# Performance work log

Measured on AMD Instinct MI355X. Metric: run time of the kernel, lower is better.

Reference implementation:

```python
import jax, jax.numpy as jnp
import numpy as np

DIM = 1024
NUM_HEADS = 16
HEAD_DIM = DIM // NUM_HEADS
ROPE_THETA = 10000.0
SCALE = HEAD_DIM ** -0.5


def _apply_rope(x, cos, sin):
    # x: [B, H, S, head_dim]; cos/sin: [S, head_dim//2] (broadcast over B, H)
    x_even = x[..., 0::2]
    x_odd = x[..., 1::2]
    rot_even = x_even * cos - x_odd * sin
    rot_odd = x_even * sin + x_odd * cos
    # interleave back: stack on last axis then flatten, matching torch .stack(-1).flatten(-2)
    return jnp.stack([rot_even, rot_odd], axis=-1).reshape(x.shape)


def setup_inputs() -> dict:
    key = jax.random.key(0)
    k0, k1, k2 = jax.random.split(key, 3)
    B, S = 2, 2048
    x = jax.random.normal(k0, (B, S, DIM), dtype=jnp.float32)
    # small_init: std = sqrt(2 / (5*dim))
    qkv_w = jax.random.normal(k1, (3 * DIM, DIM), dtype=jnp.float32) * (2.0 / (5 * DIM)) ** 0.5
    qkv_b = jnp.zeros((3 * DIM,), dtype=jnp.float32)
    # wang_init: std = 2 / num_blocks / sqrt(dim) scaled
    out_w = jax.random.normal(k2, (DIM, DIM), dtype=jnp.float32) * (2.0 / DIM) ** 0.5 / 2.0
    out_b = jnp.zeros((DIM,), dtype=jnp.float32)
    return {"x": x, "qkv_w": qkv_w, "qkv_b": qkv_b, "out_w": out_w, "out_b": out_b, "window_size": 512}


def reference(x, qkv_w, qkv_b, out_w, out_b, window_size):
    B, S, D = x.shape
    qkv = x @ qkv_w.T + qkv_b                          # [B, S, 3D]
    qkv = qkv.reshape(B, S, 3, NUM_HEADS, HEAD_DIM).transpose(2, 0, 3, 1, 4)
    q, k, v = qkv[0], qkv[1], qkv[2]                   # each [B, H, S, hd]

    pos = jnp.arange(S, dtype=jnp.float32)
    inv_freq = 1.0 / (ROPE_THETA ** (jnp.arange(0, HEAD_DIM, 2, dtype=jnp.float32) / HEAD_DIM))
    freqs = pos[:, None] * inv_freq                    # [S, hd//2]
    cos, sin = jnp.cos(freqs), jnp.sin(freqs)
    q = _apply_rope(q, cos, sin)
    k = _apply_rope(k, cos, sin)

    scores = jnp.einsum('bhqd,bhkd->bhqk', q, k) * SCALE
    i = jnp.arange(S)
    mask = (i[:, None] >= i[None, :]) & ((i[:, None] - i[None, :]) < window_size)  # causal sliding window
    scores = jnp.where(mask, scores, -jnp.inf)
    attn = jax.nn.softmax(scores, axis=-1)
    out = jnp.einsum('bhqk,bhkd->bhqd', attn, v)       # [B, H, S, hd]
    out = out.transpose(0, 2, 1, 3).reshape(B, S, D)
    return out @ out_w.T + out_b
```

## Files before the change

kernel.cpp:

```cpp
#include <hip/hip_runtime.h>
#include <hip/hip_bf16.h>
#include <cstdint>
#include <cstddef>

using bf16x8 = __attribute__((ext_vector_type(8))) short;
using f32x4  = __attribute__((ext_vector_type(4))) float;

#define MFMA16(a, b, c) __builtin_amdgcn_mfma_f32_16x16x32_bf16((a), (b), (c), 0, 0, 0)

__device__ __forceinline__ unsigned short f2bf(float f) {
    unsigned int u = __float_as_uint(f);
    u += 0x7fffu + ((u >> 16) & 1u);
    return (unsigned short)(u >> 16);
}
__device__ __forceinline__ uint32_t pack2bf(float a, float b) {
    __hip_bfloat162 h = __float22bfloat162_rn(float2{a, b});
    return *(uint32_t*)&h;
}
__device__ __forceinline__ float bf2f(short x) {
    return __uint_as_float(((uint32_t)(unsigned short)x) << 16);
}

__device__ __forceinline__ void gload_lds16(const void* g, void* l) {
    __builtin_amdgcn_global_load_lds(
        (const __attribute__((address_space(1))) void*)g,
        (__attribute__((address_space(3))) void*)l, 16, 0, 0);
}

#define S_LEN 2048
#define NHEAD 16
#define HDIM  64
#define DIM   1024
#define WIN   512
#define MROWS 4096

__global__ void prep(float* __restrict__ cosT, float* __restrict__ sinT,
                     const float* __restrict__ x, unsigned short* __restrict__ xb,
                     const float* __restrict__ qw, unsigned short* __restrict__ qwb,
                     const float* __restrict__ ow, unsigned short* __restrict__ owb) {
    int t = blockIdx.x * 256 + threadIdx.x;
    if (t < 65536) {
        int s = t >> 5, f = t & 31;
        float invf = powf(10000.0f, -(float)f / 32.0f);
        float ang = (float)s * invf;
        cosT[t] = cosf(ang);
        sinT[t] = sinf(ang);
        return;
    }
    int u = t - 65536;
    const float* src;
    unsigned short* dst;
    int i;
    if (u < 1048576)        { src = x;  dst = xb;  i = u * 4; }
    else if (u < 1835008)   { src = qw; dst = qwb; i = (u - 1048576) * 4; }
    else                    { src = ow; dst = owb; i = (u - 1835008) * 4; }
    float4 v = *(const float4*)(src + i);
    ushort4 o;
    o.x = f2bf(v.x); o.y = f2bf(v.y); o.z = f2bf(v.z); o.w = f2bf(v.w);
    *(ushort4*)(dst + i) = o;
}

__global__ __launch_bounds__(256) void gemm_qkv_fused(
        const unsigned short* __restrict__ A,
        const unsigned short* __restrict__ Bw,
        const float* __restrict__ bias,
        const float* __restrict__ cosT, const float* __restrict__ sinT,
        unsigned short* __restrict__ qbuf,
        unsigned short* __restrict__ kbuf,
        unsigned short* __restrict__ vtb) {
    __shared__ __align__(16) char smem_raw[34816];
    const int tid = threadIdx.x;
    const int lane = tid & 63, w = tid >> 6;
    const int wr = w >> 1, wc = w & 1, lm = lane & 15, lg = lane >> 4;
    const int bx = blockIdx.x, by = blockIdx.y;
    const int row0 = by * 128, col0 = bx * 128;
    const int plane = bx >> 3;
    const int h0 = (bx & 7) * 2;
    const int b = by >> 4, s_base = (by & 15) * 128;

    f32x4 acc[4][4];
#pragma unroll
    for (int m = 0; m < 4; ++m)
#pragma unroll
        for (int n = 0; n < 4; ++n) acc[m][n] = (f32x4){0.f, 0.f, 0.f, 0.f};

    short* As = (short*)smem_raw;
    short* Bs = (short*)(smem_raw + 16384);

    for (int kt = 0; kt < 16; ++kt) {
#pragma unroll
        for (int i = 0; i < 4; ++i) {
            int c = tid + 256 * i;
            int r = c >> 3, gs = (c & 7) ^ (r & 7);
            gload_lds16((const char*)A  + (size_t)(row0 + r) * 2048 + (size_t)kt * 128 + gs * 16, As + c * 8);
            gload_lds16((const char*)Bw + (size_t)(col0 + r) * 2048 + (size_t)kt * 128 + gs * 16, Bs + c * 8);
        }
        __syncthreads();
        bf16x8 af0[4], af1[4], bf0[4], bf1[4];
#pragma unroll
        for (int m = 0; m < 4; ++m) {
            int rl = wr * 64 + m * 16 + lm, rb = rl & 7;
            af0[m] = *(const bf16x8*)&As[rl * 64 + ((lg ^ rb) << 3)];
            af1[m] = *(const bf16x8*)&As[rl * 64 + (((lg + 4) ^ rb) << 3)];
        }
#pragma unroll
        for (int n = 0; n < 4; ++n) {
            int rl = wc * 64 + n * 16 + lm, rb = rl & 7;
            bf0[n] = *(const bf16x8*)&Bs[rl * 64 + ((lg ^ rb) << 3)];
            bf1[n] = *(const bf16x8*)&Bs[rl * 64 + (((lg + 4) ^ rb) << 3)];
        }
#pragma unroll
        for (int m = 0; m < 4; ++m)
#pragma unroll
            for (int n = 0; n < 4; ++n) {
                acc[m][n] = MFMA16(af0[m], bf0[n], acc[m][n]);
                acc[m][n] = MFMA16(af1[m], bf1[n], acc[m][n]);
            }
        __syncthreads();
    }

    unsigned short (*tile)[136] = (unsigned short(*)[136])smem_raw;
    const int lane8 = tid & 7, idx = tid >> 3;

    if (plane < 2) {
#pragma unroll
        for (int m = 0; m < 4; ++m)
#pragma unroll
            for (int n = 0; n < 4; ++n) {
                int colL = wc * 64 + n * 16 + lm;
                float bv = bias[col0 + colL];
#pragma unroll
                for (int r = 0; r < 4; ++r)
                    tile[wr * 64 + m * 16 + lg * 4 + r][colL] = f2bf(acc[m][n][r] + bv);
            }
    } else {
#pragma unroll
        for (int m = 0; m < 4; ++m)
#pragma unroll
            for (int n = 0; n < 4; ++n) {
                int colL = wc * 64 + n * 16 + lm;
                float bv = bias[col0 + colL];
                uint2 pk;
                pk.x = pack2bf(acc[m][n][0] + bv, acc[m][n][1] + bv);
                pk.y = pack2bf(acc[m][n][2] + bv, acc[m][n][3] + bv);
                *(uint2*)&tile[colL][wr * 64 + m * 16 + lg * 4] = pk;
            }
    }
    __syncthreads();

    if (plane < 2) {
        unsigned short* dstp = (plane == 0) ? qbuf : kbuf;
        const float qsc = (plane == 0) ? 0.125f : 1.0f;
        int d0 = lane8 * 8;
#pragma unroll
        for (int j = 0; j < 4; ++j) {
            int srow = idx + 32 * j;
            int s = s_base + srow;
            float4 c4 = *(const float4*)&cosT[s * 32 + (d0 >> 1)];
            float4 s4 = *(const float4*)&sinT[s * 32 + (d0 >> 1)];
#pragma unroll
            for (int hh = 0; hh < 2; ++hh) {
                bf16x8 v = *(const bf16x8*)&tile[srow][hh * 64 + d0];
                float e0 = bf2f(v[0]), o0 = bf2f(v[1]);
                float e1 = bf2f(v[2]), o1 = bf2f(v[3]);
                float e2 = bf2f(v[4]), o2 = bf2f(v[5]);
                float e3 = bf2f(v[6]), o3 = bf2f(v[7]);
                uint4 pk;
                pk.x = pack2bf((e0 * c4.x - o0 * s4.x) * qsc, (e0 * s4.x + o0 * c4.x) * qsc);
                pk.y = pack2bf((e1 * c4.y - o1 * s4.y) * qsc, (e1 * s4.y + o1 * c4.y) * qsc);
                pk.z = pack2bf((e2 * c4.z - o2 * s4.z) * qsc, (e2 * s4.z + o2 * c4.z) * qsc);
                pk.w = pack2bf((e3 * c4.w - o3 * s4.w) * qsc, (e3 * s4.w + o3 * c4.w) * qsc);
                int h = h0 + hh;
                *(uint4*)&dstp[(((size_t)(b * NHEAD + h)) * S_LEN + s) * 64 + d0] = pk;
            }
        }
    } else {
#pragma unroll
        for (int rr = 0; rr < 4; ++rr) {
            int hd = rr * 32 + idx;
            int hh = hd >> 6, d = hd & 63, h = h0 + hh;
#pragma unroll
            for (int j = 0; j < 2; ++j) {
                int s0 = lane8 * 8 + j * 64;
                bf16x8 v = *(const bf16x8*)&tile[hd][s0];
                *(bf16x8*)&vtb[((size_t)(b * NHEAD + h) * 64 + d) * S_LEN +
                               s_base + s0] = v;
            }
        }
    }
}

__global__ __launch_bounds__(256) void gemm_out(const unsigned short* __restrict__ A,
                                                const unsigned short* __restrict__ Bw,
                                                const float* __restrict__ bias,
                                                float* __restrict__ Cout) {
    __shared__ __align__(16) char smem_raw[24576];
    const int tid = threadIdx.x;
    const int lane = tid & 63, w = tid >> 6;
    const int wr = w >> 1, wc = w & 1, lm = lane & 15, lg = lane >> 4;
    const int row0 = blockIdx.y * 128, col0 = blockIdx.x * 64;

    f32x4 acc[4][2];
#pragma unroll
    for (int m = 0; m < 4; ++m)
#pragma unroll
        for (int n = 0; n < 2; ++n) acc[m][n] = (f32x4){0.f, 0.f, 0.f, 0.f};

    short* As = (short*)smem_raw;
    short* Bs = (short*)(smem_raw + 16384);

    for (int kt = 0; kt < 16; ++kt) {
#pragma unroll
        for (int i = 0; i < 4; ++i) {
            int c = tid + 256 * i;
            int r = c >> 3, gs = (c & 7) ^ (r & 7);
            gload_lds16((const char*)A + (size_t)(row0 + r) * 2048 + (size_t)kt * 128 + gs * 16, As + c * 8);
        }
#pragma unroll
        for (int i = 0; i < 2; ++i) {
            int c = tid + 256 * i;
            int r = c >> 3, gs = (c & 7) ^ (r & 7);
            gload_lds16((const char*)Bw + (size_t)(col0 + r) * 2048 + (size_t)kt * 128 + gs * 16, Bs + c * 8);
        }
        __syncthreads();
        bf16x8 af0[4], af1[4], bf0[2], bf1[2];
#pragma unroll
        for (int m = 0; m < 4; ++m) {
            int rl = wr * 64 + m * 16 + lm, rb = rl & 7;
            af0[m] = *(const bf16x8*)&As[rl * 64 + ((lg ^ rb) << 3)];
            af1[m] = *(const bf16x8*)&As[rl * 64 + (((lg + 4) ^ rb) << 3)];
        }
#pragma unroll
        for (int n = 0; n < 2; ++n) {
            int rl = wc * 32 + n * 16 + lm, rb = rl & 7;
            bf0[n] = *(const bf16x8*)&Bs[rl * 64 + ((lg ^ rb) << 3)];
            bf1[n] = *(const bf16x8*)&Bs[rl * 64 + (((lg + 4) ^ rb) << 3)];
        }
#pragma unroll
        for (int m = 0; m < 4; ++m)
#pragma unroll
            for (int n = 0; n < 2; ++n) {
                acc[m][n] = MFMA16(af0[m], bf0[n], acc[m][n]);
                acc[m][n] = MFMA16(af1[m], bf1[n], acc[m][n]);
            }
        __syncthreads();
    }

#pragma unroll
    for (int m = 0; m < 4; ++m) {
        int row = row0 + wr * 64 + m * 16 + lg * 4;
#pragma unroll
        for (int n = 0; n < 2; ++n) {
            int col = col0 + wc * 32 + n * 16 + lm;
            float bv = bias[col];
#pragma unroll
            for (int r = 0; r < 4; ++r)
                Cout[(size_t)(row + r) * DIM + col] = acc[m][n][r] + bv;
        }
    }
}

__global__ __launch_bounds__(256) void attn(const unsigned short* __restrict__ qb,
                                            const unsigned short* __restrict__ kb,
                                            const unsigned short* __restrict__ vt,
                                            unsigned short* __restrict__ ao) {
    const int p = blockIdx.x;
    const int L = (p & 7) * 128 + (p >> 3);
    const int qblk = L & 31, bh = L >> 5;
    const int b = bh >> 4, h = bh & 15;
    const int tid = threadIdx.x, w = tid >> 6, lane = tid & 63;
    const int lm = lane & 15, lg = lane >> 4;
    const unsigned short* Qb = qb + (size_t)bh * S_LEN * 64;
    const unsigned short* Kb = kb + (size_t)bh * S_LEN * 64;
    const unsigned short* Vt = vt + (size_t)bh * 64 * S_LEN;
    const int q0 = qblk * 64 + w * 16;

    __shared__ short Ks[2][64 * 64];
    __shared__ short Plds[4][16 * 64];
    short* Pw = Plds[w];

    bf16x8 aq0 = *(const bf16x8*)&Qb[(q0 + lm) * 64 + lg * 8];
    bf16x8 aq1 = *(const bf16x8*)&Qb[(q0 + lm) * 64 + lg * 8 + 32];

    f32x4 o[4];
#pragma unroll
    for (int n = 0; n < 4; ++n) o[n] = (f32x4){0.f, 0.f, 0.f, 0.f};
    float lsum = 0.f;

    const int qq = q0 + lm;
    const int t0 = qblk >= 8 ? qblk - 8 : 0;

    auto stage = [&](int kt, int buf) {
#pragma unroll
        for (int i = 0; i < 2; ++i) {
            int c = tid + 256 * i;
            int r = c >> 3, g = (c & 7) ^ (r & 7);
            gload_lds16(Kb + (size_t)(kt * 64 + r) * 64 + g * 8, &Ks[buf][c * 8]);
        }
    };

    stage(t0, 0);
    __syncthreads();
    int cur = 0;
    const int sw = lm & 7;
    for (int kt = t0; kt <= qblk; ++kt) {
        if (kt < qblk) stage(kt + 1, cur ^ 1);
        const int kbase = kt * 64;
        f32x4 sT[4];
        __builtin_amdgcn_s_setprio(1);
#pragma unroll
        for (int n = 0; n < 4; ++n) {
            int rl = n * 16 + lm;
            bf16x8 bk0 = *(const bf16x8*)&Ks[cur][rl * 64 + ((lg ^ sw) << 3)];
            bf16x8 bk1 = *(const bf16x8*)&Ks[cur][rl * 64 + (((lg + 4) ^ sw) << 3)];
            f32x4 z = (f32x4){0.f, 0.f, 0.f, 0.f};
            z = MFMA16(bk0, aq0, z);
            sT[n] = MFMA16(bk1, aq1, z);
        }
        __builtin_amdgcn_s_setprio(0);
#pragma unroll
        for (int n = 0; n < 4; ++n) {
            int kk0 = kbase + n * 16 + lg * 4;
#pragma unroll
            for (int r = 0; r < 4; ++r) {
                int d = qq - (kk0 + r);
                float pv = ((unsigned)d < (unsigned)WIN) ? __expf(sT[n][r]) : 0.f;
                sT[n][r] = pv;
                lsum += pv;
            }
            uint2 pk;
            pk.x = pack2bf(sT[n][0], sT[n][1]);
            pk.y = pack2bf(sT[n][2], sT[n][3]);
            *(uint2*)&Pw[lm * 64 + ((((2 * n + (lg >> 1)) ^ sw) << 3) + ((lg & 1) << 2))] = pk;
        }
        bf16x8 ap0 = *(const bf16x8*)&Pw[lm * 64 + ((lg ^ sw) << 3)];
        bf16x8 ap1 = *(const bf16x8*)&Pw[lm * 64 + (((lg + 4) ^ sw) << 3)];
        __builtin_amdgcn_s_setprio(1);
#pragma unroll
        for (int n = 0; n < 4; ++n) {
            bf16x8 bv0 = *(const bf16x8*)&Vt[(size_t)(n * 16 + lm) * S_LEN + kbase + lg * 8];
            bf16x8 bv1 = *(const bf16x8*)&Vt[(size_t)(n * 16 + lm) * S_LEN + kbase + lg * 8 + 32];
            o[n] = MFMA16(ap0, bv0, o[n]);
            o[n] = MFMA16(ap1, bv1, o[n]);
        }
        __builtin_amdgcn_s_setprio(0);
        __syncthreads();
        cur ^= 1;
    }
    lsum += __shfl_xor(lsum, 16, 64);
    lsum += __shfl_xor(lsum, 32, 64);
    float linv = 1.f / lsum;
    float lrow[4];
#pragma unroll
    for (int r = 0; r < 4; ++r) lrow[r] = __shfl(linv, lg * 4 + r, 64);
#pragma unroll
    for (int n = 0; n < 4; ++n)
#pragma unroll
        for (int r = 0; r < 4; ++r) {
            int row = b * S_LEN + q0 + lg * 4 + r;
            int col = h * 64 + n * 16 + lm;
            ao[(size_t)row * DIM + col] = f2bf(o[n][r] * lrow[r]);
        }
}

extern "C" void kernel_launch(void* const* d_in, const int* in_sizes, int n_in,
                              void* d_out, int out_size, void* d_ws, size_t ws_size,
                              hipStream_t stream) {
    const float* x      = (const float*)d_in[0];
    const float* qkv_w  = (const float*)d_in[1];
    const float* qkv_b  = (const float*)d_in[2];
    const float* out_w  = (const float*)d_in[3];
    const float* out_b  = (const float*)d_in[4];
    (void)in_sizes; (void)n_in; (void)out_size; (void)ws_size;

    char* ws = (char*)d_ws;
    float*          cosT = (float*)(ws + 0);
    float*          sinT = (float*)(ws + 262144);
    unsigned short* xb   = (unsigned short*)(ws + 524288);
    unsigned short* wqb  = (unsigned short*)(ws + 8912896);
    unsigned short* owb  = (unsigned short*)(ws + 15204352);
    unsigned short* qbuf = (unsigned short*)(ws + 17301504);
    unsigned short* kbuf = (unsigned short*)(ws + 25690112);
    unsigned short* vtb  = (unsigned short*)(ws + 34078720);
    unsigned short* aob  = (unsigned short*)(ws + 42467328);

    prep<<<8448, 256, 0, stream>>>(cosT, sinT, x, xb, qkv_w, wqb, out_w, owb);

    gemm_qkv_fused<<<dim3(24, 32), 256, 0, stream>>>(xb, wqb, qkv_b, cosT, sinT,
                                                     qbuf, kbuf, vtb);

    attn<<<1024, 256, 0, stream>>>(qbuf, kbuf, vtb, aob);

    gemm_out<<<dim3(16, 32), 256, 0, stream>>>(aob, owb, out_b, (float*)d_out);
}
```

Measured before the change: 115.0 us.

## Stage K and V in 128-key LDS tiles and swizzle GEMM block order

The attention kernel now loads 128-key tiles of both K and V^T into LDS with a single sync, instead of double-buffered 64-key K tiles plus direct global V reads. Each tile is processed as two 64-key halves, and halves outside the sliding window are skipped. This is meant to cut scattered global V loads and halve the number of barriers, but it gives up the prefetch overlap and may load unused keys at the window edges. Both GEMM kernels also remap block indices into an interleaved order, aiming for better L2 reuse.

```diff
diff --git a/kernel.cpp b/kernel.cpp
--- a/kernel.cpp
+++ b/kernel.cpp
@@ -72,7 +72,9 @@
     const int tid = threadIdx.x;
     const int lane = tid & 63, w = tid >> 6;
     const int wr = w >> 1, wc = w & 1, lm = lane & 15, lg = lane >> 4;
-    const int bx = blockIdx.x, by = blockIdx.y;
+    const int lin = blockIdx.y * 24 + blockIdx.x;
+    const int Lr = (lin & 7) * 96 + (lin >> 3);
+    const int bx = Lr % 24, by = Lr / 24;
     const int row0 = by * 128, col0 = bx * 128;
     const int plane = bx >> 3;
     const int h0 = (bx & 7) * 2;
@@ -198,7 +200,10 @@
     const int tid = threadIdx.x;
     const int lane = tid & 63, w = tid >> 6;
     const int wr = w >> 1, wc = w & 1, lm = lane & 15, lg = lane >> 4;
-    const int row0 = blockIdx.y * 128, col0 = blockIdx.x * 64;
+    const int lin = blockIdx.y * 16 + blockIdx.x;
+    const int Lr = (lin & 7) * 64 + (lin >> 3);
+    const int bx = Lr & 15, by = Lr >> 4;
+    const int row0 = by * 128, col0 = bx * 64;
 
     f32x4 acc[4][2];
 #pragma unroll
@@ -275,7 +280,8 @@
     const unsigned short* Vt = vt + (size_t)bh * 64 * S_LEN;
     const int q0 = qblk * 64 + w * 16;
 
-    __shared__ short Ks[2][64 * 64];
+    __shared__ short Ks[128 * 64];
+    __shared__ short Vs[64 * 128];
     __shared__ short Plds[4][16 * 64];
     short* Pw = Plds[w];
 
@@ -288,64 +294,70 @@
     float lsum = 0.f;
 
     const int qq = q0 + lm;
-    const int t0 = qblk >= 8 ? qblk - 8 : 0;
-
-    auto stage = [&](int kt, int buf) {
-#pragma unroll
-        for (int i = 0; i < 2; ++i) {
+    const int t0_64 = qblk >= 8 ? qblk - 8 : 0;
+    const int first = t0_64 >> 1, last = qblk >> 1;
+    const int sw = lm & 7;
+
+    for (int kt = first; kt <= last; ++kt) {
+#pragma unroll
+        for (int i = 0; i < 4; ++i) {
             int c = tid + 256 * i;
             int r = c >> 3, g = (c & 7) ^ (r & 7);
-            gload_lds16(Kb + (size_t)(kt * 64 + r) * 64 + g * 8, &Ks[buf][c * 8]);
-        }
-    };
-
-    stage(t0, 0);
-    __syncthreads();
-    int cur = 0;
-    const int sw = lm & 7;
-    for (int kt = t0; kt <= qblk; ++kt) {
-        if (kt < qblk) stage(kt + 1, cur ^ 1);
-        const int kbase = kt * 64;
-        f32x4 sT[4];
-        __builtin_amdgcn_s_setprio(1);
-#pragma unroll
-        for (int n = 0; n < 4; ++n) {
-            int rl = n * 16 + lm;
-            bf16x8 bk0 = *(const bf16x8*)&Ks[cur][rl * 64 + ((lg ^ sw) << 3)];
-            bf16x8 bk1 = *(const bf16x8*)&Ks[cur][rl * 64 + (((lg + 4) ^ sw) << 3)];
-            f32x4 z = (f32x4){0.f, 0.f, 0.f, 0.f};
-            z = MFMA16(bk0, aq0, z);
-            sT[n] = MFMA16(bk1, aq1, z);
-        }
-        __builtin_amdgcn_s_setprio(0);
-#pragma unroll
-        for (int n = 0; n < 4; ++n) {
-            int kk0 = kbase + n * 16 + lg * 4;
-#pragma unroll
-            for (int r = 0; r < 4; ++r) {
-                int d = qq - (kk0 + r);
-                float pv = ((unsigned)d < (unsigned)WIN) ? __expf(sT[n][r]) : 0.f;
-                sT[n][r] = pv;
-                lsum += pv;
-            }
-            uint2 pk;
-            pk.x = pack2bf(sT[n][0], sT[n][1]);
-            pk.y = pack2bf(sT[n][2], sT[n][3]);
-            *(uint2*)&Pw[lm * 64 + ((((2 * n + (lg >> 1)) ^ sw) << 3) + ((lg & 1) << 2))] = pk;
-        }
-        bf16x8 ap0 = *(const bf16x8*)&Pw[lm * 64 + ((lg ^ sw) << 3)];
-        bf16x8 ap1 = *(const bf16x8*)&Pw[lm * 64 + (((lg + 4) ^ sw) << 3)];
-        __builtin_amdgcn_s_setprio(1);
-#pragma unroll
-        for (int n = 0; n < 4; ++n) {
-            bf16x8 bv0 = *(const bf16x8*)&Vt[(size_t)(n * 16 + lm) * S_LEN + kbase + lg * 8];
-            bf16x8 bv1 = *(const bf16x8*)&Vt[(size_t)(n * 16 + lm) * S_LEN + kbase + lg * 8 + 32];
-            o[n] = MFMA16(ap0, bv0, o[n]);
-            o[n] = MFMA16(ap1, bv1, o[n]);
-        }
-        __builtin_amdgcn_s_setprio(0);
-        __syncthreads();
-        cur ^= 1;
+            gload_lds16(Kb + (size_t)(kt * 128 + r) * 64 + g * 8, &Ks[c * 8]);
+        }
+#pragma unroll
+        for (int i = 0; i < 4; ++i) {
+            int c = tid + 256 * i;
+            int r = c >> 4, g = (c & 15) ^ (r & 7);
+            gload_lds16(Vt + (size_t)r * S_LEN + kt * 128 + g * 8, &Vs[c * 8]);
+        }
+        __syncthreads();
+#pragma unroll
+        for (int half = 0; half < 2; ++half) {
+            const int h64 = kt * 2 + half;
+            if (h64 < t0_64 || h64 > qblk) continue;
+            const int kbase = h64 * 64;
+            f32x4 sT[4];
+            __builtin_amdgcn_s_setprio(1);
+#pragma unroll
+            for (int n = 0; n < 4; ++n) {
+                int rl = half * 64 + n * 16 + lm;
+                bf16x8 bk0 = *(const bf16x8*)&Ks[rl * 64 + ((lg ^ sw) << 3)];
+                bf16x8 bk1 = *(const bf16x8*)&Ks[rl * 64 + (((lg + 4) ^ sw) << 3)];
+                f32x4 z = (f32x4){0.f, 0.f, 0.f, 0.f};
+                z = MFMA16(bk0, aq0, z);
+                sT[n] = MFMA16(bk1, aq1, z);
+            }
+            __builtin_amdgcn_s_setprio(0);
+#pragma unroll
+            for (int n = 0; n < 4; ++n) {
+                int kk0 = kbase + n * 16 + lg * 4;
+#pragma unroll
+                for (int r = 0; r < 4; ++r) {
+                    int d = qq - (kk0 + r);
+                    float pv = ((unsigned)d < (unsigned)WIN) ? __expf(sT[n][r]) : 0.f;
+                    sT[n][r] = pv;
+                    lsum += pv;
+                }
+                uint2 pk;
+                pk.x = pack2bf(sT[n][0], sT[n][1]);
+                pk.y = pack2bf(sT[n][2], sT[n][3]);
+                *(uint2*)&Pw[lm * 64 + ((((2 * n + (lg >> 1)) ^ sw) << 3) + ((lg & 1) << 2))] = pk;
+            }
+            bf16x8 ap0 = *(const bf16x8*)&Pw[lm * 64 + ((lg ^ sw) << 3)];
+            bf16x8 ap1 = *(const bf16x8*)&Pw[lm * 64 + (((lg + 4) ^ sw) << 3)];
+            __builtin_amdgcn_s_setprio(1);
+#pragma unroll
+            for (int n = 0; n < 4; ++n) {
+                int rl = n * 16 + lm;
+                bf16x8 bv0 = *(const bf16x8*)&Vs[rl * 128 + half * 64 + ((lg ^ sw) << 3)];
+                bf16x8 bv1 = *(const bf16x8*)&Vs[rl * 128 + half * 64 + (((lg + 4) ^ sw) << 3)];
+                o[n] = MFMA16(ap0, bv0, o[n]);
+                o[n] = MFMA16(ap1, bv1, o[n]);
+            }
+            __builtin_amdgcn_s_setprio(0);
+        }
+        __syncthreads();
     }
     lsum += __shfl_xor(lsum, 16, 64);
     lsum += __shfl_xor(lsum, 32, 64);
```

After: 96.00 us. 1.2x faster.
